# Performance work log

Measured on AMD Instinct MI355X. Metric: run time of the kernel, lower is better.

## Reference

```python
import jax, jax.numpy as jnp
import numpy as np

N_NODES = 100000
N_EDGES = 1600000
N_FEAT = 64
HIDDEN = 64
N_GRAPHS = 64
N_CLASSES = 2


def setup_inputs() -> dict:
    key = jax.random.key(0)
    ks = jax.random.split(key, 12)
    x = jax.random.normal(ks[0], (N_NODES, N_FEAT), dtype=jnp.float32)
    edge_index = jax.random.randint(ks[1], (2, N_EDGES), 0, N_NODES, dtype=jnp.int32)
    batch = jnp.sort(jax.random.randint(ks[2], (N_NODES,), 0, N_GRAPHS, dtype=jnp.int32))
    # Glorot-style init for GCNConv weights, zeros for biases (PyG default)
    def glorot(k, fan_in, fan_out):
        s = jnp.sqrt(6.0 / (fan_in + fan_out))
        return jax.random.uniform(k, (fan_in, fan_out), jnp.float32, -s, s)
    W1 = glorot(ks[3], N_FEAT, HIDDEN); b1 = jnp.zeros((HIDDEN,), jnp.float32)
    W2 = glorot(ks[4], HIDDEN, HIDDEN); b2 = jnp.zeros((HIDDEN,), jnp.float32)
    W3 = glorot(ks[5], HIDDEN, HIDDEN); b3 = jnp.zeros((HIDDEN,), jnp.float32)
    Wl = glorot(ks[6], HIDDEN, N_CLASSES); bl = jnp.zeros((N_CLASSES,), jnp.float32)
    return {"x": x, "edge_index": edge_index, "batch": batch,
            "W1": W1, "b1": b1, "W2": W2, "b2": b2, "W3": W3, "b3": b3,
            "Wl": Wl, "bl": bl}


def _gcn_conv(h, W, b, src, dst, dinv, n_nodes):
    # GCNConv with self-loops: out_i = sum_j d_i^-1/2 d_j^-1/2 (x_j W) + d_i^-1 (x_i W) + b
    h = h @ W                                   # [N, H]
    coef = (dinv[src] * dinv[dst])[:, None]     # [E, 1]
    agg = jax.ops.segment_sum(coef * h[src], dst, num_segments=n_nodes)
    return agg + (dinv * dinv)[:, None] * h + b


def reference(x, edge_index, batch, W1, b1, W2, b2, W3, b3, Wl, bl):
    src, dst = edge_index[0], edge_index[1]
    # degree of A + I (edge weight 1), shared by all three convs
    deg = jax.ops.segment_sum(jnp.ones((N_EDGES,), x.dtype), dst, num_segments=N_NODES) + 1.0
    dinv = jax.lax.rsqrt(deg)

    h = jax.nn.relu(_gcn_conv(x, W1, b1, src, dst, dinv, N_NODES))
    h = jax.nn.relu(_gcn_conv(h, W2, b2, src, dst, dinv, N_NODES))
    h = _gcn_conv(h, W3, b3, src, dst, dinv, N_NODES)

    # global_mean_pool over graph ids
    sums = jax.ops.segment_sum(h, batch, num_segments=N_GRAPHS)
    cnts = jax.ops.segment_sum(jnp.ones((N_NODES,), x.dtype), batch, num_segments=N_GRAPHS)
    pooled = sums / jnp.maximum(cnts, 1.0)[:, None]

    # dropout(p=0.5) is identity in eval mode
    return pooled @ Wl + bl
```

## Files before the change

kernel.cpp:

```cpp
#include <hip/hip_runtime.h>


#define NF 64
#define ELLW 64
#define BINSHIFT 9
#define BINW 512
#define NB 196
#define BINCAP 9216
#define LPITCH 68

typedef __attribute__((ext_vector_type(8))) short bf16x8;
typedef __attribute__((ext_vector_type(4))) float f32x4;

__device__ inline float bf2f(unsigned short u) {
    return __uint_as_float(((unsigned int)u) << 16);
}
__device__ inline float bf2f_lo(unsigned int u) {
    return __uint_as_float(u << 16);
}
__device__ inline float bf2f_hi(unsigned int u) {
    return __uint_as_float(u & 0xFFFF0000u);
}
__device__ inline unsigned short f2bf(float f) {
    unsigned int u = __float_as_uint(f);
    u = (u + 0x7fff + ((u >> 16) & 1)) >> 16;
    return (unsigned short)u;
}

__global__ void binA_kernel(const int* __restrict__ src, const int* __restrict__ dst,
                            int* __restrict__ binCnt, int* __restrict__ binEdges,
                            int nE, int chunk) {
    __shared__ int hist[NB];
    __shared__ int base[NB];
    int t = threadIdx.x;
    if (t < NB) hist[t] = 0;
    __syncthreads();
    int e0 = blockIdx.x * chunk;
    int e1 = min(e0 + chunk, nE);
    for (int e = e0 + t; e < e1; e += blockDim.x) {
        int b = dst[e] >> BINSHIFT;
        atomicAdd(&hist[b], 1);
    }
    __syncthreads();
    if (t < NB) {
        base[t] = atomicAdd(&binCnt[t], hist[t]);
        hist[t] = 0;
    }
    __syncthreads();
    for (int e = e0 + t; e < e1; e += blockDim.x) {
        int d = dst[e];
        int b = d >> BINSHIFT;
        int pos = base[b] + atomicAdd(&hist[b], 1);
        if (pos < BINCAP)
            binEdges[(size_t)b * BINCAP + pos] = src[e] | ((d & (BINW - 1)) << 17);
    }
}

__global__ void __launch_bounds__(512) binB_kernel(const int* __restrict__ binEdges,
                            const int* __restrict__ binCnt, int* __restrict__ cnt,
                            float* __restrict__ dinv, int* __restrict__ colELL, int n,
                            unsigned int* __restrict__ dummyA, unsigned int* __restrict__ dummyB) {
    __shared__ int lcnt[BINW];
    int t = threadIdx.x;
    int b = blockIdx.x;
    if (b == 0 && t < 32) { dummyA[t] = 0u; dummyB[t] = 0u; }
    for (int i = t; i < BINW; i += blockDim.x) lcnt[i] = 1;
    __syncthreads();
    int m = binCnt[b];
    if (m > BINCAP) m = BINCAP;
    const int* be = binEdges + (size_t)b * BINCAP;
    int nbase = b << BINSHIFT;
    for (int e = t; e < m; e += blockDim.x) {
        int v = be[e];
        int s = v & 0x1FFFF;
        int dl = v >> 17;
        int pos = atomicAdd(&lcnt[dl], 1);
        if (pos < ELLW) colELL[(size_t)(nbase + dl) * ELLW + pos] = s;
    }
    __syncthreads();
    for (int i = t; i < BINW; i += blockDim.x) {
        int node = nbase + i;
        if (node < n) {
            int c = lcnt[i];
            if (c > ELLW) c = ELLW;
            colELL[(size_t)node * ELLW + 0] = node;
            int cpad = (c + 3) & ~3;
            for (int j = c; j < cpad; ++j)
                colELL[(size_t)node * ELLW + j] = n;
            cnt[node] = c;
            dinv[node] = rsqrtf((float)c);
        }
    }
}

__device__ inline void load_W_frags(const float* __restrict__ W, int r16, int kq,
                                    bf16x8 bfr[4][2]) {
#pragma unroll
    for (int nt = 0; nt < 4; ++nt)
#pragma unroll
        for (int kh = 0; kh < 2; ++kh) {
            bf16x8 f;
#pragma unroll
            for (int j = 0; j < 8; ++j)
                f[j] = (short)f2bf(W[(kh * 32 + kq * 8 + j) * NF + nt * 16 + r16]);
            bfr[nt][kh] = f;
        }
}

__global__ void __launch_bounds__(256) gemm1_mfma_kernel(const float* __restrict__ A,
                                                         const float* __restrict__ W,
                                                         const float* __restrict__ dinv,
                                                         unsigned short* __restrict__ outB, int n) {
    __shared__ unsigned short T[4][16 * LPITCH];
    int lane = threadIdx.x & 63;
    int r16 = lane & 15, kq = lane >> 4;
    int wv = threadIdx.x >> 6;
    int wid = blockIdx.x * 4 + wv;
    int nw = gridDim.x * 4;
    bf16x8 bfr[4][2];
    load_W_frags(W, r16, kq, bfr);
    int ntiles = n >> 4;
    for (int t = wid; t < ntiles; t += nw) {
        int r0 = t << 4;
        const float* ar = A + (size_t)(r0 + r16) * NF + kq * 8;
        bf16x8 a0, a1;
        float4 v0 = *(const float4*)(ar);
        float4 v1 = *(const float4*)(ar + 4);
        float4 v2 = *(const float4*)(ar + 32);
        float4 v3 = *(const float4*)(ar + 36);
        a0[0] = (short)f2bf(v0.x); a0[1] = (short)f2bf(v0.y);
        a0[2] = (short)f2bf(v0.z); a0[3] = (short)f2bf(v0.w);
        a0[4] = (short)f2bf(v1.x); a0[5] = (short)f2bf(v1.y);
        a0[6] = (short)f2bf(v1.z); a0[7] = (short)f2bf(v1.w);
        a1[0] = (short)f2bf(v2.x); a1[1] = (short)f2bf(v2.y);
        a1[2] = (short)f2bf(v2.z); a1[3] = (short)f2bf(v2.w);
        a1[4] = (short)f2bf(v3.x); a1[5] = (short)f2bf(v3.y);
        a1[6] = (short)f2bf(v3.z); a1[7] = (short)f2bf(v3.w);
        f32x4 acc[4];
#pragma unroll
        for (int nt = 0; nt < 4; ++nt) {
            acc[nt] = (f32x4)(0.0f);
            acc[nt] = __builtin_amdgcn_mfma_f32_16x16x32_bf16(a0, bfr[nt][0], acc[nt], 0, 0, 0);
            acc[nt] = __builtin_amdgcn_mfma_f32_16x16x32_bf16(a1, bfr[nt][1], acc[nt], 0, 0, 0);
        }
        float ds[4];
#pragma unroll
        for (int reg = 0; reg < 4; ++reg) ds[reg] = dinv[r0 + kq * 4 + reg];
        unsigned short* Tw = T[wv];
#pragma unroll
        for (int nt = 0; nt < 4; ++nt)
#pragma unroll
            for (int reg = 0; reg < 4; ++reg)
                Tw[(kq * 4 + reg) * LPITCH + nt * 16 + r16] = f2bf(acc[nt][reg] * ds[reg]);
#pragma unroll
        for (int it = 0; it < 4; ++it) {
            int row = it * 4 + kq;
            uint2 v = *(const uint2*)&Tw[row * LPITCH + r16 * 4];
            *(uint2*)(outB + (size_t)(r0 + row) * NF + r16 * 4) = v;
        }
    }
}

__global__ void __launch_bounds__(256) fused_agg_gemm_kernel(
        const unsigned short* __restrict__ hB, const int* __restrict__ colELL,
        const int* __restrict__ cnt, const float* __restrict__ dinv,
        const float* __restrict__ bias, const float* __restrict__ W,
        unsigned short* __restrict__ outB, int n) {
    __shared__ int Icol[16 * 32];
    __shared__ int Icnt[16];
    __shared__ unsigned short Tin[2048];
    __shared__ unsigned short Tout[16 * LPITCH];
    int lane = threadIdx.x & 63;
    int wv = threadIdx.x >> 6;
    int es = lane >> 4, fq = lane & 15;
    int r16 = lane & 15, kq = lane >> 4;
    int r0 = blockIdx.x << 4;
    if (threadIdx.x < 128) {
        int srow = threadIdx.x >> 3, sj = threadIdx.x & 7;
        ((int4*)Icol)[srow * 8 + sj] =
            *(const int4*)(colELL + (size_t)(r0 + srow) * ELLW + sj * 4);
    } else if (threadIdx.x < 144) {
        Icnt[threadIdx.x - 128] = cnt[r0 + threadIdx.x - 128];
    }
    bf16x8 bfr0, bfr1;
    {
        bf16x8 f0, f1;
#pragma unroll
        for (int j = 0; j < 8; ++j) {
            f0[j] = (short)f2bf(W[(kq * 8 + j) * NF + wv * 16 + r16]);
            f1[j] = (short)f2bf(W[(32 + kq * 8 + j) * NF + wv * 16 + r16]);
        }
        bfr0 = f0; bfr1 = f1;
    }
    __syncthreads();
#pragma unroll
    for (int rr = 0; rr < 4; ++rr) {
        int lrow = wv * 4 + rr;
        int row = r0 + lrow;
        int c = Icnt[lrow];
        int nq = (c + 3) >> 2;
        int nqL = nq < 8 ? nq : 8;
        const int* cr = Icol + lrow * 32;
        float a0 = 0.f, a1 = 0.f, a2 = 0.f, a3 = 0.f;
        int q = 0;
        for (; q + 4 <= nqL; q += 4) {
            int s0 = cr[q * 4 + es];
            int s1 = cr[q * 4 + 4 + es];
            int s2 = cr[q * 4 + 8 + es];
            int s3 = cr[q * 4 + 12 + es];
            uint2 u0 = *(const uint2*)(hB + (size_t)s0 * NF + fq * 4);
            uint2 u1 = *(const uint2*)(hB + (size_t)s1 * NF + fq * 4);
            uint2 u2 = *(const uint2*)(hB + (size_t)s2 * NF + fq * 4);
            uint2 u3 = *(const uint2*)(hB + (size_t)s3 * NF + fq * 4);
            a0 += (bf2f_lo(u0.x) + bf2f_lo(u1.x)) + (bf2f_lo(u2.x) + bf2f_lo(u3.x));
            a1 += (bf2f_hi(u0.x) + bf2f_hi(u1.x)) + (bf2f_hi(u2.x) + bf2f_hi(u3.x));
            a2 += (bf2f_lo(u0.y) + bf2f_lo(u1.y)) + (bf2f_lo(u2.y) + bf2f_lo(u3.y));
            a3 += (bf2f_hi(u0.y) + bf2f_hi(u1.y)) + (bf2f_hi(u2.y) + bf2f_hi(u3.y));
        }
        for (; q + 2 <= nqL; q += 2) {
            int s0 = cr[q * 4 + es];
            int s1 = cr[q * 4 + 4 + es];
            uint2 u0 = *(const uint2*)(hB + (size_t)s0 * NF + fq * 4);
            uint2 u1 = *(const uint2*)(hB + (size_t)s1 * NF + fq * 4);
            a0 += bf2f_lo(u0.x) + bf2f_lo(u1.x);
            a1 += bf2f_hi(u0.x) + bf2f_hi(u1.x);
            a2 += bf2f_lo(u0.y) + bf2f_lo(u1.y);
            a3 += bf2f_hi(u0.y) + bf2f_hi(u1.y);
        }
        if (q < nqL) {
            int s0 = cr[q * 4 + es];
            uint2 u0 = *(const uint2*)(hB + (size_t)s0 * NF + fq * 4);
            a0 += bf2f_lo(u0.x); a1 += bf2f_hi(u0.x);
            a2 += bf2f_lo(u0.y); a3 += bf2f_hi(u0.y);
        }
        if (nq > 8) {
            const int* crg = colELL + (size_t)row * ELLW;
            for (int qq = 8; qq < nq; ++qq) {
                int s0 = crg[qq * 4 + es];
                uint2 u0 = *(const uint2*)(hB + (size_t)s0 * NF + fq * 4);
                a0 += bf2f_lo(u0.x); a1 += bf2f_hi(u0.x);
                a2 += bf2f_lo(u0.y); a3 += bf2f_hi(u0.y);
            }
        }
        a0 += __shfl_xor(a0, 16); a1 += __shfl_xor(a1, 16);
        a2 += __shfl_xor(a2, 16); a3 += __shfl_xor(a3, 16);
        a0 += __shfl_xor(a0, 32); a1 += __shfl_xor(a1, 32);
        a2 += __shfl_xor(a2, 32); a3 += __shfl_xor(a3, 32);
        if (es == 0) {
            float dd = dinv[row];
            float4 b4 = *(const float4*)(bias + fq * 4);
            a0 = fmaxf(dd * a0 + b4.x, 0.f); a1 = fmaxf(dd * a1 + b4.y, 0.f);
            a2 = fmaxf(dd * a2 + b4.z, 0.f); a3 = fmaxf(dd * a3 + b4.w, 0.f);
            uint2 v;
            v.x = (unsigned int)f2bf(a0) | ((unsigned int)f2bf(a1) << 16);
            v.y = (unsigned int)f2bf(a2) | ((unsigned int)f2bf(a3) << 16);
            int ibase = ((fq >> 3) << 10) + (((fq >> 1) & 3) << 7)
                      + (wv * 4 + rr) * 8 + ((fq & 1) << 2);
            *(uint2*)&Tin[ibase] = v;
        }
    }
    __syncthreads();
    bf16x8 A0 = *(const bf16x8*)&Tin[lane * 8];
    bf16x8 A1 = *(const bf16x8*)&Tin[1024 + lane * 8];
    f32x4 acc = (f32x4)(0.0f);
    acc = __builtin_amdgcn_mfma_f32_16x16x32_bf16(A0, bfr0, acc, 0, 0, 0);
    acc = __builtin_amdgcn_mfma_f32_16x16x32_bf16(A1, bfr1, acc, 0, 0, 0);
    float ds[4];
#pragma unroll
    for (int reg = 0; reg < 4; ++reg) ds[reg] = dinv[r0 + kq * 4 + reg];
#pragma unroll
    for (int reg = 0; reg < 4; ++reg)
        Tout[(kq * 4 + reg) * LPITCH + wv * 16 + r16] = f2bf(acc[reg] * ds[reg]);
    __syncthreads();
    int t = threadIdx.x;
    int orow = t >> 4, ocq = t & 15;
    uint2 v = *(const uint2*)&Tout[orow * LPITCH + ocq * 4];
    *(uint2*)(outB + (size_t)(r0 + orow) * NF + ocq * 4) = v;
}

__global__ void __launch_bounds__(256) gather3_kernel(
        const unsigned short* __restrict__ hB, const int* __restrict__ colELL,
        const int* __restrict__ cnt, const float* __restrict__ dinv,
        const float* __restrict__ bias, unsigned short* __restrict__ outB, int n) {
    __shared__ int Icol[16 * 32];
    __shared__ int Icnt[16];
    int lane = threadIdx.x & 63;
    int wv = threadIdx.x >> 6;
    int es = lane >> 4, fq = lane & 15;
    int r0 = blockIdx.x << 4;
    if (threadIdx.x < 128) {
        int srow = threadIdx.x >> 3, sj = threadIdx.x & 7;
        ((int4*)Icol)[srow * 8 + sj] =
            *(const int4*)(colELL + (size_t)(r0 + srow) * ELLW + sj * 4);
    } else if (threadIdx.x < 144) {
        Icnt[threadIdx.x - 128] = cnt[r0 + threadIdx.x - 128];
    }
    __syncthreads();
    float4 b4 = *(const float4*)(bias + fq * 4);
#pragma unroll
    for (int rr = 0; rr < 4; ++rr) {
        int lrow = wv * 4 + rr;
        int row = r0 + lrow;
        int c = Icnt[lrow];
        int nq = (c + 3) >> 2;
        int nqL = nq < 8 ? nq : 8;
        const int* cr = Icol + lrow * 32;
        float a0 = 0.f, a1 = 0.f, a2 = 0.f, a3 = 0.f;
        int q = 0;
        for (; q + 4 <= nqL; q += 4) {
            int s0 = cr[q * 4 + es];
            int s1 = cr[q * 4 + 4 + es];
            int s2 = cr[q * 4 + 8 + es];
            int s3 = cr[q * 4 + 12 + es];
            uint2 u0 = *(const uint2*)(hB + (size_t)s0 * NF + fq * 4);
            uint2 u1 = *(const uint2*)(hB + (size_t)s1 * NF + fq * 4);
            uint2 u2 = *(const uint2*)(hB + (size_t)s2 * NF + fq * 4);
            uint2 u3 = *(const uint2*)(hB + (size_t)s3 * NF + fq * 4);
            a0 += (bf2f_lo(u0.x) + bf2f_lo(u1.x)) + (bf2f_lo(u2.x) + bf2f_lo(u3.x));
            a1 += (bf2f_hi(u0.x) + bf2f_hi(u1.x)) + (bf2f_hi(u2.x) + bf2f_hi(u3.x));
            a2 += (bf2f_lo(u0.y) + bf2f_lo(u1.y)) + (bf2f_lo(u2.y) + bf2f_lo(u3.y));
            a3 += (bf2f_hi(u0.y) + bf2f_hi(u1.y)) + (bf2f_hi(u2.y) + bf2f_hi(u3.y));
        }
        for (; q + 2 <= nqL; q += 2) {
            int s0 = cr[q * 4 + es];
            int s1 = cr[q * 4 + 4 + es];
            uint2 u0 = *(const uint2*)(hB + (size_t)s0 * NF + fq * 4);
            uint2 u1 = *(const uint2*)(hB + (size_t)s1 * NF + fq * 4);
            a0 += bf2f_lo(u0.x) + bf2f_lo(u1.x);
            a1 += bf2f_hi(u0.x) + bf2f_hi(u1.x);
            a2 += bf2f_lo(u0.y) + bf2f_lo(u1.y);
            a3 += bf2f_hi(u0.y) + bf2f_hi(u1.y);
        }
        if (q < nqL) {
            int s0 = cr[q * 4 + es];
            uint2 u0 = *(const uint2*)(hB + (size_t)s0 * NF + fq * 4);
            a0 += bf2f_lo(u0.x); a1 += bf2f_hi(u0.x);
            a2 += bf2f_lo(u0.y); a3 += bf2f_hi(u0.y);
        }
        if (nq > 8) {
            const int* crg = colELL + (size_t)row * ELLW;
            for (int qq = 8; qq < nq; ++qq) {
                int s0 = crg[qq * 4 + es];
                uint2 u0 = *(const uint2*)(hB + (size_t)s0 * NF + fq * 4);
                a0 += bf2f_lo(u0.x); a1 += bf2f_hi(u0.x);
                a2 += bf2f_lo(u0.y); a3 += bf2f_hi(u0.y);
            }
        }
        a0 += __shfl_xor(a0, 16); a1 += __shfl_xor(a1, 16);
        a2 += __shfl_xor(a2, 16); a3 += __shfl_xor(a3, 16);
        a0 += __shfl_xor(a0, 32); a1 += __shfl_xor(a1, 32);
        a2 += __shfl_xor(a2, 32); a3 += __shfl_xor(a3, 32);
        if (es == 0) {
            float dd = dinv[row];
            float r0f = dd * a0 + b4.x, r1f = dd * a1 + b4.y;
            float r2f = dd * a2 + b4.z, r3f = dd * a3 + b4.w;
            uint2 v;
            v.x = (unsigned int)f2bf(r0f) | ((unsigned int)f2bf(r1f) << 16);
            v.y = (unsigned int)f2bf(r2f) | ((unsigned int)f2bf(r3f) << 16);
            *(uint2*)(outB + (size_t)row * NF + fq * 4) = v;
        }
    }
}

__global__ void __launch_bounds__(256) pool_kernel(const unsigned short* __restrict__ hB,
                            const int* __restrict__ batch,
                            float* __restrict__ pooled, int n) {
    const int CHUNK = 32;
    int wave = blockIdx.x * 4 + (threadIdx.x >> 6);
    int lane = threadIdx.x & 63;
    int start = wave * CHUNK;
    if (start >= n) return;
    int end = min(start + CHUNK, n);
    int gfirst = batch[start], glast = batch[end - 1];
    if (gfirst == glast && end - start == CHUNK) {
        float acc = 0.f;
#pragma unroll
        for (int r = 0; r < CHUNK; r += 8) {
            size_t base = (size_t)(start + r) * NF + lane;
            float v0 = bf2f(hB[base + 0 * NF]);
            float v1 = bf2f(hB[base + 1 * NF]);
            float v2 = bf2f(hB[base + 2 * NF]);
            float v3 = bf2f(hB[base + 3 * NF]);
            float v4 = bf2f(hB[base + 4 * NF]);
            float v5 = bf2f(hB[base + 5 * NF]);
            float v6 = bf2f(hB[base + 6 * NF]);
            float v7 = bf2f(hB[base + 7 * NF]);
            acc += ((v0 + v1) + (v2 + v3)) + ((v4 + v5) + (v6 + v7));
        }
        atomicAdd(&pooled[gfirst * NF + lane], acc);
    } else {
        int cur = gfirst;
        float acc = 0.f;
        for (int i = start; i < end; ++i) {
            int g = batch[i];
            if (g != cur) {
                atomicAdd(&pooled[cur * NF + lane], acc);
                acc = 0.f; cur = g;
            }
            acc += bf2f(hB[(size_t)i * NF + lane]);
        }
        atomicAdd(&pooled[cur * NF + lane], acc);
    }
}

__global__ void counts_kernel(const int* __restrict__ batch, float* __restrict__ counts, int n) {
    __shared__ int h[64];
    int t = threadIdx.x;
    if (t < 64) h[t] = 0;
    __syncthreads();
    for (int i = blockIdx.x * blockDim.x + t; i < n; i += gridDim.x * blockDim.x)
        atomicAdd(&h[batch[i]], 1);
    __syncthreads();
    if (t < 64 && h[t] > 0) atomicAdd(&counts[t], (float)h[t]);
}

__global__ void final_kernel(const float* __restrict__ pooled, const float* __restrict__ counts,
                             const float* __restrict__ Wl, const float* __restrict__ bl,
                             float* __restrict__ out) {
    int t = threadIdx.x;
    int g = t >> 1, c = t & 1;
    float inv = 1.0f / fmaxf(counts[g], 1.0f);
    float s = 0.0f;
#pragma unroll
    for (int j = 0; j < NF; ++j) s += pooled[g * NF + j] * Wl[j * 2 + c];
    out[t] = s * inv + bl[c];
}

extern "C" void kernel_launch(void* const* d_in, const int* in_sizes, int n_in,
                              void* d_out, int out_size, void* d_ws, size_t ws_size,
                              hipStream_t stream) {
    const float* x     = (const float*)d_in[0];
    const int*   ei    = (const int*)d_in[1];
    const int*   batch = (const int*)d_in[2];
    const float* W1    = (const float*)d_in[3];
    const float* b1    = (const float*)d_in[4];
    const float* W2    = (const float*)d_in[5];
    const float* b2    = (const float*)d_in[6];
    const float* W3    = (const float*)d_in[7];
    const float* b3    = (const float*)d_in[8];
    const float* Wl    = (const float*)d_in[9];
    const float* bl    = (const float*)d_in[10];
    float* out = (float*)d_out;

    const int n  = in_sizes[0] / NF;
    const int nE = in_sizes[1] / 2;
    const int* src = ei;
    const int* dst = ei + nE;

    char* ws = (char*)d_ws;
    auto alloc = [&](size_t bytes) {
        char* p = ws;
        ws += (bytes + 255) & ~(size_t)255;
        return p;
    };
    unsigned short* bufA = (unsigned short*)alloc((size_t)(n + 16) * NF * 2);
    unsigned short* bufB = (unsigned short*)alloc((size_t)(n + 16) * NF * 2);
    float* scratch = (float*)alloc((size_t)n * NF * 4);
    int*   binEdges = (int*)scratch;
    int*   colELL = (int*)alloc((size_t)n * ELLW * 4);
    float* dinv   = (float*)alloc((size_t)(n + 16) * 4);
    int*   cnt    = (int*)alloc((size_t)n * 4);
    char*  ztail  = ws;
    int*   binCnt = (int*)alloc(NB * 4);
    float* pooled = (float*)alloc(64 * NF * 4);
    float* counts = (float*)alloc(64 * 4);
    size_t zbytes = (size_t)(ws - ztail);

    hipMemsetAsync(ztail, 0, zbytes, stream);

    const int chunk = 3200;
    binA_kernel<<<(nE + chunk - 1) / chunk, 256, 0, stream>>>(src, dst, binCnt, binEdges, nE, chunk);
    binB_kernel<<<NB, 512, 0, stream>>>(binEdges, binCnt, cnt, dinv, colELL, n,
                                        (unsigned int*)(bufA + (size_t)n * NF),
                                        (unsigned int*)(bufB + (size_t)n * NF));
    counts_kernel<<<98, 1024, 0, stream>>>(batch, counts, n);

    const int tile_grid = n >> 4;

    gemm1_mfma_kernel<<<1563, 256, 0, stream>>>(x, W1, dinv, bufA, n);
    fused_agg_gemm_kernel<<<tile_grid, 256, 0, stream>>>(bufA, colELL, cnt, dinv, b1, W2, bufB, n);
    fused_agg_gemm_kernel<<<tile_grid, 256, 0, stream>>>(bufB, colELL, cnt, dinv, b2, W3, bufA, n);
    gather3_kernel<<<tile_grid, 256, 0, stream>>>(bufA, colELL, cnt, dinv, b3, bufB, n);

    pool_kernel<<<(n / 32 + 3) / 4, 256, 0, stream>>>(bufB, batch, pooled, n);
    final_kernel<<<1, 128, 0, stream>>>(pooled, counts, Wl, bl, out);
}
```

Before: 261.9 us.

## Switch intermediates to fp16, pre-convert weights, fuse layer-3 gather with pooling

Replaces bf16 storage and MFMA with fp16 across all layers, summing gathered neighbour rows with packed half adds before widening to float. A small prep kernel converts W1-W3 to fp16 once, so the GEMM kernels no longer round weights per block. The final gather kernel now accumulates the mean-pool sums directly through shared-memory and global atomics, which removes the layer-3 output write and the separate pool pass. The trade-off is reduced fp16 range and precision for partial sums, plus contention on the pooling atomics.

```diff
diff --git a/kernel.cpp b/kernel.cpp
--- a/kernel.cpp
+++ b/kernel.cpp
@@ -9,22 +9,16 @@
 #define BINCAP 9216
 #define LPITCH 68
 
-typedef __attribute__((ext_vector_type(8))) short bf16x8;
+typedef __attribute__((ext_vector_type(8))) _Float16 f16x8;
+typedef __attribute__((ext_vector_type(4))) _Float16 f16x4;
 typedef __attribute__((ext_vector_type(4))) float f32x4;
 
-__device__ inline float bf2f(unsigned short u) {
-    return __uint_as_float(((unsigned int)u) << 16);
-}
-__device__ inline float bf2f_lo(unsigned int u) {
-    return __uint_as_float(u << 16);
-}
-__device__ inline float bf2f_hi(unsigned int u) {
-    return __uint_as_float(u & 0xFFFF0000u);
-}
-__device__ inline unsigned short f2bf(float f) {
-    unsigned int u = __float_as_uint(f);
-    u = (u + 0x7fff + ((u >> 16) & 1)) >> 16;
-    return (unsigned short)u;
+__device__ inline unsigned short f2h_u(float f) {
+    return __builtin_bit_cast(unsigned short, (_Float16)f);
+}
+__device__ inline unsigned int pack_h2(float a, float b) {
+    unsigned int ua = f2h_u(a), ub = f2h_u(b);
+    return ua | (ub << 16);
 }
 
 __global__ void binA_kernel(const int* __restrict__ src, const int* __restrict__ dst,
@@ -93,22 +87,34 @@
     }
 }
 
-__device__ inline void load_W_frags(const float* __restrict__ W, int r16, int kq,
-                                    bf16x8 bfr[4][2]) {
+__global__ void prep_kernel(const float* __restrict__ W1, const float* __restrict__ W2,
+                            const float* __restrict__ W3, unsigned short* __restrict__ w1h,
+                            unsigned short* __restrict__ w2h, unsigned short* __restrict__ w3h) {
+    int t = blockIdx.x * blockDim.x + threadIdx.x;
+    if (t < NF * NF) {
+        w1h[t] = f2h_u(W1[t]);
+        w2h[t] = f2h_u(W2[t]);
+        w3h[t] = f2h_u(W3[t]);
+    }
+}
+
+__device__ inline void load_W_frags(const unsigned short* __restrict__ Wh, int r16, int kq,
+                                    f16x8 bfr[4][2]) {
 #pragma unroll
     for (int nt = 0; nt < 4; ++nt)
 #pragma unroll
         for (int kh = 0; kh < 2; ++kh) {
-            bf16x8 f;
+            f16x8 f;
 #pragma unroll
             for (int j = 0; j < 8; ++j)
-                f[j] = (short)f2bf(W[(kh * 32 + kq * 8 + j) * NF + nt * 16 + r16]);
+                f[j] = __builtin_bit_cast(_Float16,
+                        Wh[(kh * 32 + kq * 8 + j) * NF + nt * 16 + r16]);
             bfr[nt][kh] = f;
         }
 }
 
 __global__ void __launch_bounds__(256) gemm1_mfma_kernel(const float* __restrict__ A,
-                                                         const float* __restrict__ W,
+                                                         const unsigned short* __restrict__ Wh,
                                                          const float* __restrict__ dinv,
                                                          unsigned short* __restrict__ outB, int n) {
     __shared__ unsigned short T[4][16 * LPITCH];
@@ -117,31 +123,31 @@
     int wv = threadIdx.x >> 6;
     int wid = blockIdx.x * 4 + wv;
     int nw = gridDim.x * 4;
-    bf16x8 bfr[4][2];
-    load_W_frags(W, r16, kq, bfr);
+    f16x8 bfr[4][2];
+    load_W_frags(Wh, r16, kq, bfr);
     int ntiles = n >> 4;
     for (int t = wid; t < ntiles; t += nw) {
         int r0 = t << 4;
         const float* ar = A + (size_t)(r0 + r16) * NF + kq * 8;
-        bf16x8 a0, a1;
+        f16x8 a0, a1;
         float4 v0 = *(const float4*)(ar);
         float4 v1 = *(const float4*)(ar + 4);
         float4 v2 = *(const float4*)(ar + 32);
         float4 v3 = *(const float4*)(ar + 36);
-        a0[0] = (short)f2bf(v0.x); a0[1] = (short)f2bf(v0.y);
-        a0[2] = (short)f2bf(v0.z); a0[3] = (short)f2bf(v0.w);
-        a0[4] = (short)f2bf(v1.x); a0[5] = (short)f2bf(v1.y);
-        a0[6] = (short)f2bf(v1.z); a0[7] = (short)f2bf(v1.w);
-        a1[0] = (short)f2bf(v2.x); a1[1] = (short)f2bf(v2.y);
-        a1[2] = (short)f2bf(v2.z); a1[3] = (short)f2bf(v2.w);
-        a1[4] = (short)f2bf(v3.x); a1[5] = (short)f2bf(v3.y);
-        a1[6] = (short)f2bf(v3.z); a1[7] = (short)f2bf(v3.w);
+        a0[0] = (_Float16)v0.x; a0[1] = (_Float16)v0.y;
+        a0[2] = (_Float16)v0.z; a0[3] = (_Float16)v0.w;
+        a0[4] = (_Float16)v1.x; a0[5] = (_Float16)v1.y;
+        a0[6] = (_Float16)v1.z; a0[7] = (_Float16)v1.w;
+        a1[0] = (_Float16)v2.x; a1[1] = (_Float16)v2.y;
+        a1[2] = (_Float16)v2.z; a1[3] = (_Float16)v2.w;
+        a1[4] = (_Float16)v3.x; a1[5] = (_Float16)v3.y;
+        a1[6] = (_Float16)v3.z; a1[7] = (_Float16)v3.w;
         f32x4 acc[4];
 #pragma unroll
         for (int nt = 0; nt < 4; ++nt) {
             acc[nt] = (f32x4)(0.0f);
-            acc[nt] = __builtin_amdgcn_mfma_f32_16x16x32_bf16(a0, bfr[nt][0], acc[nt], 0, 0, 0);
-            acc[nt] = __builtin_amdgcn_mfma_f32_16x16x32_bf16(a1, bfr[nt][1], acc[nt], 0, 0, 0);
+            acc[nt] = __builtin_amdgcn_mfma_f32_16x16x32_f16(a0, bfr[nt][0], acc[nt], 0, 0, 0);
+            acc[nt] = __builtin_amdgcn_mfma_f32_16x16x32_f16(a1, bfr[nt][1], acc[nt], 0, 0, 0);
         }
         float ds[4];
 #pragma unroll
@@ -151,7 +157,7 @@
         for (int nt = 0; nt < 4; ++nt)
 #pragma unroll
             for (int reg = 0; reg < 4; ++reg)
-                Tw[(kq * 4 + reg) * LPITCH + nt * 16 + r16] = f2bf(acc[nt][reg] * ds[reg]);
+                Tw[(kq * 4 + reg) * LPITCH + nt * 16 + r16] = f2h_u(acc[nt][reg] * ds[reg]);
 #pragma unroll
         for (int it = 0; it < 4; ++it) {
             int row = it * 4 + kq;
@@ -164,7 +170,7 @@
 __global__ void __launch_bounds__(256) fused_agg_gemm_kernel(
         const unsigned short* __restrict__ hB, const int* __restrict__ colELL,
         const int* __restrict__ cnt, const float* __restrict__ dinv,
-        const float* __restrict__ bias, const float* __restrict__ W,
+        const float* __restrict__ bias, const unsigned short* __restrict__ Wh,
         unsigned short* __restrict__ outB, int n) {
     __shared__ int Icol[16 * 32];
     __shared__ int Icnt[16];
@@ -182,13 +188,13 @@
     } else if (threadIdx.x < 144) {
         Icnt[threadIdx.x - 128] = cnt[r0 + threadIdx.x - 128];
     }
-    bf16x8 bfr0, bfr1;
+    f16x8 bfr0, bfr1;
     {
-        bf16x8 f0, f1;
+        f16x8 f0, f1;
 #pragma unroll
         for (int j = 0; j < 8; ++j) {
-            f0[j] = (short)f2bf(W[(kq * 8 + j) * NF + wv * 16 + r16]);
-            f1[j] = (short)f2bf(W[(32 + kq * 8 + j) * NF + wv * 16 + r16]);
+            f0[j] = __builtin_bit_cast(_Float16, Wh[(kq * 8 + j) * NF + wv * 16 + r16]);
+            f1[j] = __builtin_bit_cast(_Float16, Wh[(32 + kq * 8 + j) * NF + wv * 16 + r16]);
         }
         bfr0 = f0; bfr1 = f1;
     }
@@ -208,38 +214,36 @@
             int s1 = cr[q * 4 + 4 + es];
             int s2 = cr[q * 4 + 8 + es];
             int s3 = cr[q * 4 + 12 + es];
-            uint2 u0 = *(const uint2*)(hB + (size_t)s0 * NF + fq * 4);
-            uint2 u1 = *(const uint2*)(hB + (size_t)s1 * NF + fq * 4);
-            uint2 u2 = *(const uint2*)(hB + (size_t)s2 * NF + fq * 4);
-            uint2 u3 = *(const uint2*)(hB + (size_t)s3 * NF + fq * 4);
-            a0 += (bf2f_lo(u0.x) + bf2f_lo(u1.x)) + (bf2f_lo(u2.x) + bf2f_lo(u3.x));
-            a1 += (bf2f_hi(u0.x) + bf2f_hi(u1.x)) + (bf2f_hi(u2.x) + bf2f_hi(u3.x));
-            a2 += (bf2f_lo(u0.y) + bf2f_lo(u1.y)) + (bf2f_lo(u2.y) + bf2f_lo(u3.y));
-            a3 += (bf2f_hi(u0.y) + bf2f_hi(u1.y)) + (bf2f_hi(u2.y) + bf2f_hi(u3.y));
+            f16x4 h0 = __builtin_bit_cast(f16x4, *(const uint2*)(hB + (size_t)s0 * NF + fq * 4));
+            f16x4 h1 = __builtin_bit_cast(f16x4, *(const uint2*)(hB + (size_t)s1 * NF + fq * 4));
+            f16x4 h2 = __builtin_bit_cast(f16x4, *(const uint2*)(hB + (size_t)s2 * NF + fq * 4));
+            f16x4 h3 = __builtin_bit_cast(f16x4, *(const uint2*)(hB + (size_t)s3 * NF + fq * 4));
+            f16x4 tt = (h0 + h1) + (h2 + h3);
+            a0 += (float)tt[0]; a1 += (float)tt[1];
+            a2 += (float)tt[2]; a3 += (float)tt[3];
         }
         for (; q + 2 <= nqL; q += 2) {
             int s0 = cr[q * 4 + es];
             int s1 = cr[q * 4 + 4 + es];
-            uint2 u0 = *(const uint2*)(hB + (size_t)s0 * NF + fq * 4);
-            uint2 u1 = *(const uint2*)(hB + (size_t)s1 * NF + fq * 4);
-            a0 += bf2f_lo(u0.x) + bf2f_lo(u1.x);
-            a1 += bf2f_hi(u0.x) + bf2f_hi(u1.x);
-            a2 += bf2f_lo(u0.y) + bf2f_lo(u1.y);
-            a3 += bf2f_hi(u0.y) + bf2f_hi(u1.y);
+            f16x4 h0 = __builtin_bit_cast(f16x4, *(const uint2*)(hB + (size_t)s0 * NF + fq * 4));
+            f16x4 h1 = __builtin_bit_cast(f16x4, *(const uint2*)(hB + (size_t)s1 * NF + fq * 4));
+            f16x4 tt = h0 + h1;
+            a0 += (float)tt[0]; a1 += (float)tt[1];
+            a2 += (float)tt[2]; a3 += (float)tt[3];
         }
         if (q < nqL) {
             int s0 = cr[q * 4 + es];
-            uint2 u0 = *(const uint2*)(hB + (size_t)s0 * NF + fq * 4);
-            a0 += bf2f_lo(u0.x); a1 += bf2f_hi(u0.x);
-            a2 += bf2f_lo(u0.y); a3 += bf2f_hi(u0.y);
+            f16x4 h0 = __builtin_bit_cast(f16x4, *(const uint2*)(hB + (size_t)s0 * NF + fq * 4));
+            a0 += (float)h0[0]; a1 += (float)h0[1];
+            a2 += (float)h0[2]; a3 += (float)h0[3];
         }
         if (nq > 8) {
             const int* crg = colELL + (size_t)row * ELLW;
             for (int qq = 8; qq < nq; ++qq) {
                 int s0 = crg[qq * 4 + es];
-                uint2 u0 = *(const uint2*)(hB + (size_t)s0 * NF + fq * 4);
-                a0 += bf2f_lo(u0.x); a1 += bf2f_hi(u0.x);
-                a2 += bf2f_lo(u0.y); a3 += bf2f_hi(u0.y);
+                f16x4 h0 = __builtin_bit_cast(f16x4, *(const uint2*)(hB + (size_t)s0 * NF + fq * 4));
+                a0 += (float)h0[0]; a1 += (float)h0[1];
+                a2 += (float)h0[2]; a3 += (float)h0[3];
             }
         }
         a0 += __shfl_xor(a0, 16); a1 += __shfl_xor(a1, 16);
@@ -252,25 +256,25 @@
             a0 = fmaxf(dd * a0 + b4.x, 0.f); a1 = fmaxf(dd * a1 + b4.y, 0.f);
             a2 = fmaxf(dd * a2 + b4.z, 0.f); a3 = fmaxf(dd * a3 + b4.w, 0.f);
             uint2 v;
-            v.x = (unsigned int)f2bf(a0) | ((unsigned int)f2bf(a1) << 16);
-            v.y = (unsigned int)f2bf(a2) | ((unsigned int)f2bf(a3) << 16);
+            v.x = pack_h2(a0, a1);
+            v.y = pack_h2(a2, a3);
             int ibase = ((fq >> 3) << 10) + (((fq >> 1) & 3) << 7)
                       + (wv * 4 + rr) * 8 + ((fq & 1) << 2);
             *(uint2*)&Tin[ibase] = v;
         }
     }
     __syncthreads();
-    bf16x8 A0 = *(const bf16x8*)&Tin[lane * 8];
-    bf16x8 A1 = *(const bf16x8*)&Tin[1024 + lane * 8];
+    f16x8 A0 = *(const f16x8*)&Tin[lane * 8];
+    f16x8 A1 = *(const f16x8*)&Tin[1024 + lane * 8];
     f32x4 acc = (f32x4)(0.0f);
-    acc = __builtin_amdgcn_mfma_f32_16x16x32_bf16(A0, bfr0, acc, 0, 0, 0);
-    acc = __builtin_amdgcn_mfma_f32_16x16x32_bf16(A1, bfr1, acc, 0, 0, 0);
+    acc = __builtin_amdgcn_mfma_f32_16x16x32_f16(A0, bfr0, acc, 0, 0, 0);
+    acc = __builtin_amdgcn_mfma_f32_16x16x32_f16(A1, bfr1, acc, 0, 0, 0);
     float ds[4];
 #pragma unroll
     for (int reg = 0; reg < 4; ++reg) ds[reg] = dinv[r0 + kq * 4 + reg];
 #pragma unroll
     for (int reg = 0; reg < 4; ++reg)
-        Tout[(kq * 4 + reg) * LPITCH + wv * 16 + r16] = f2bf(acc[reg] * ds[reg]);
+        Tout[(kq * 4 + reg) * LPITCH + wv * 16 + r16] = f2h_u(acc[reg] * ds[reg]);
     __syncthreads();
     int t = threadIdx.x;
     int orow = t >> 4, ocq = t & 15;
@@ -278,12 +282,14 @@
     *(uint2*)(outB + (size_t)(r0 + orow) * NF + ocq * 4) = v;
 }
 
-__global__ void __launch_bounds__(256) gather3_kernel(
+__global__ void __launch_bounds__(256) gather3_pool_kernel(
         const unsigned short* __restrict__ hB, const int* __restrict__ colELL,
         const int* __restrict__ cnt, const float* __restrict__ dinv,
-        const float* __restrict__ bias, unsigned short* __restrict__ outB, int n) {
+        const float* __restrict__ bias, const int* __restrict__ batch,
+        float* __restrict__ pooled, int n) {
     __shared__ int Icol[16 * 32];
     __shared__ int Icnt[16];
+    __shared__ float PL[2][NF];
     int lane = threadIdx.x & 63;
     int wv = threadIdx.x >> 6;
     int es = lane >> 4, fq = lane & 15;
@@ -292,10 +298,12 @@
         int srow = threadIdx.x >> 3, sj = threadIdx.x & 7;
         ((int4*)Icol)[srow * 8 + sj] =
             *(const int4*)(colELL + (size_t)(r0 + srow) * ELLW + sj * 4);
+        PL[threadIdx.x >> 6][threadIdx.x & 63] = 0.f;
     } else if (threadIdx.x < 144) {
         Icnt[threadIdx.x - 128] = cnt[r0 + threadIdx.x - 128];
     }
     __syncthreads();
+    int gb = batch[r0];
     float4 b4 = *(const float4*)(bias + fq * 4);
 #pragma unroll
     for (int rr = 0; rr < 4; ++rr) {
@@ -312,38 +320,36 @@
             int s1 = cr[q * 4 + 4 + es];
             int s2 = cr[q * 4 + 8 + es];
             int s3 = cr[q * 4 + 12 + es];
-            uint2 u0 = *(const uint2*)(hB + (size_t)s0 * NF + fq * 4);
-            uint2 u1 = *(const uint2*)(hB + (size_t)s1 * NF + fq * 4);
-            uint2 u2 = *(const uint2*)(hB + (size_t)s2 * NF + fq * 4);
-            uint2 u3 = *(const uint2*)(hB + (size_t)s3 * NF + fq * 4);
-            a0 += (bf2f_lo(u0.x) + bf2f_lo(u1.x)) + (bf2f_lo(u2.x) + bf2f_lo(u3.x));
-            a1 += (bf2f_hi(u0.x) + bf2f_hi(u1.x)) + (bf2f_hi(u2.x) + bf2f_hi(u3.x));
-            a2 += (bf2f_lo(u0.y) + bf2f_lo(u1.y)) + (bf2f_lo(u2.y) + bf2f_lo(u3.y));
-            a3 += (bf2f_hi(u0.y) + bf2f_hi(u1.y)) + (bf2f_hi(u2.y) + bf2f_hi(u3.y));
+            f16x4 h0 = __builtin_bit_cast(f16x4, *(const uint2*)(hB + (size_t)s0 * NF + fq * 4));
+            f16x4 h1 = __builtin_bit_cast(f16x4, *(const uint2*)(hB + (size_t)s1 * NF + fq * 4));
+            f16x4 h2 = __builtin_bit_cast(f16x4, *(const uint2*)(hB + (size_t)s2 * NF + fq * 4));
+            f16x4 h3 = __builtin_bit_cast(f16x4, *(const uint2*)(hB + (size_t)s3 * NF + fq * 4));
+            f16x4 tt = (h0 + h1) + (h2 + h3);
+            a0 += (float)tt[0]; a1 += (float)tt[1];
+            a2 += (float)tt[2]; a3 += (float)tt[3];
         }
         for (; q + 2 <= nqL; q += 2) {
             int s0 = cr[q * 4 + es];
             int s1 = cr[q * 4 + 4 + es];
-            uint2 u0 = *(const uint2*)(hB + (size_t)s0 * NF + fq * 4);
-            uint2 u1 = *(const uint2*)(hB + (size_t)s1 * NF + fq * 4);
-            a0 += bf2f_lo(u0.x) + bf2f_lo(u1.x);
-            a1 += bf2f_hi(u0.x) + bf2f_hi(u1.x);
-            a2 += bf2f_lo(u0.y) + bf2f_lo(u1.y);
-            a3 += bf2f_hi(u0.y) + bf2f_hi(u1.y);
+            f16x4 h0 = __builtin_bit_cast(f16x4, *(const uint2*)(hB + (size_t)s0 * NF + fq * 4));
+            f16x4 h1 = __builtin_bit_cast(f16x4, *(const uint2*)(hB + (size_t)s1 * NF + fq * 4));
+            f16x4 tt = h0 + h1;
+            a0 += (float)tt[0]; a1 += (float)tt[1];
+            a2 += (float)tt[2]; a3 += (float)tt[3];
         }
         if (q < nqL) {
             int s0 = cr[q * 4 + es];
-            uint2 u0 = *(const uint2*)(hB + (size_t)s0 * NF + fq * 4);
-            a0 += bf2f_lo(u0.x); a1 += bf2f_hi(u0.x);
-            a2 += bf2f_lo(u0.y); a3 += bf2f_hi(u0.y);
+            f16x4 h0 = __builtin_bit_cast(f16x4, *(const uint2*)(hB + (size_t)s0 * NF + fq * 4));
+            a0 += (float)h0[0]; a1 += (float)h0[1];
+            a2 += (float)h0[2]; a3 += (float)h0[3];
         }
         if (nq > 8) {
             const int* crg = colELL + (size_t)row * ELLW;
             for (int qq = 8; qq < nq; ++qq) {
                 int s0 = crg[qq * 4 + es];
-                uint2 u0 = *(const uint2*)(hB + (size_t)s0 * NF + fq * 4);
-                a0 += bf2f_lo(u0.x); a1 += bf2f_hi(u0.x);
-                a2 += bf2f_lo(u0.y); a3 += bf2f_hi(u0.y);
+                f16x4 h0 = __builtin_bit_cast(f16x4, *(const uint2*)(hB + (size_t)s0 * NF + fq * 4));
+                a0 += (float)h0[0]; a1 += (float)h0[1];
+                a2 += (float)h0[2]; a3 += (float)h0[3];
             }
         }
         a0 += __shfl_xor(a0, 16); a1 += __shfl_xor(a1, 16);
@@ -354,52 +360,26 @@
             float dd = dinv[row];
             float r0f = dd * a0 + b4.x, r1f = dd * a1 + b4.y;
             float r2f = dd * a2 + b4.z, r3f = dd * a3 + b4.w;
-            uint2 v;
-            v.x = (unsigned int)f2bf(r0f) | ((unsigned int)f2bf(r1f) << 16);
-            v.y = (unsigned int)f2bf(r2f) | ((unsigned int)f2bf(r3f) << 16);
-            *(uint2*)(outB + (size_t)row * NF + fq * 4) = v;
-        }
-    }
-}
-
-__global__ void __launch_bounds__(256) pool_kernel(const unsigned short* __restrict__ hB,
-                            const int* __restrict__ batch,
-                            float* __restrict__ pooled, int n) {
-    const int CHUNK = 32;
-    int wave = blockIdx.x * 4 + (threadIdx.x >> 6);
-    int lane = threadIdx.x & 63;
-    int start = wave * CHUNK;
-    if (start >= n) return;
-    int end = min(start + CHUNK, n);
-    int gfirst = batch[start], glast = batch[end - 1];
-    if (gfirst == glast && end - start == CHUNK) {
-        float acc = 0.f;
-#pragma unroll
-        for (int r = 0; r < CHUNK; r += 8) {
-            size_t base = (size_t)(start + r) * NF + lane;
-            float v0 = bf2f(hB[base + 0 * NF]);
-            float v1 = bf2f(hB[base + 1 * NF]);
-            float v2 = bf2f(hB[base + 2 * NF]);
-            float v3 = bf2f(hB[base + 3 * NF]);
-            float v4 = bf2f(hB[base + 4 * NF]);
-            float v5 = bf2f(hB[base + 5 * NF]);
-            float v6 = bf2f(hB[base + 6 * NF]);
-            float v7 = bf2f(hB[base + 7 * NF]);
-            acc += ((v0 + v1) + (v2 + v3)) + ((v4 + v5) + (v6 + v7));
-        }
-        atomicAdd(&pooled[gfirst * NF + lane], acc);
-    } else {
-        int cur = gfirst;
-        float acc = 0.f;
-        for (int i = start; i < end; ++i) {
-            int g = batch[i];
-            if (g != cur) {
-                atomicAdd(&pooled[cur * NF + lane], acc);
-                acc = 0.f; cur = g;
+            int g = batch[row];
+            int sel = g - gb;
+            if (sel < 2) {
+                atomicAdd(&PL[sel][fq * 4 + 0], r0f);
+                atomicAdd(&PL[sel][fq * 4 + 1], r1f);
+                atomicAdd(&PL[sel][fq * 4 + 2], r2f);
+                atomicAdd(&PL[sel][fq * 4 + 3], r3f);
+            } else {
+                atomicAdd(&pooled[g * NF + fq * 4 + 0], r0f);
+                atomicAdd(&pooled[g * NF + fq * 4 + 1], r1f);
+                atomicAdd(&pooled[g * NF + fq * 4 + 2], r2f);
+                atomicAdd(&pooled[g * NF + fq * 4 + 3], r3f);
             }
-            acc += bf2f(hB[(size_t)i * NF + lane]);
-        }
-        atomicAdd(&pooled[cur * NF + lane], acc);
+        }
+    }
+    __syncthreads();
+    if (threadIdx.x < 128) {
+        int s = threadIdx.x >> 6, f = threadIdx.x & 63;
+        float v = PL[s][f];
+        if (v != 0.f) atomicAdd(&pooled[(gb + s) * NF + f], v);
     }
 }
 
@@ -460,6 +440,9 @@
     int*   colELL = (int*)alloc((size_t)n * ELLW * 4);
     float* dinv   = (float*)alloc((size_t)(n + 16) * 4);
     int*   cnt    = (int*)alloc((size_t)n * 4);
+    unsigned short* w1h = (unsigned short*)alloc((size_t)NF * NF * 2);
+    unsigned short* w2h = (unsigned short*)alloc((size_t)NF * NF * 2);
+    unsigned short* w3h = (unsigned short*)alloc((size_t)NF * NF * 2);
     char*  ztail  = ws;
     int*   binCnt = (int*)alloc(NB * 4);
     float* pooled = (float*)alloc(64 * NF * 4);
@@ -474,14 +457,14 @@
                                         (unsigned int*)(bufA + (size_t)n * NF),
                                         (unsigned int*)(bufB + (size_t)n * NF));
     counts_kernel<<<98, 1024, 0, stream>>>(batch, counts, n);
+    prep_kernel<<<16, 256, 0, stream>>>(W1, W2, W3, w1h, w2h, w3h);
 
     const int tile_grid = n >> 4;
 
-    gemm1_mfma_kernel<<<1563, 256, 0, stream>>>(x, W1, dinv, bufA, n);
-    fused_agg_gemm_kernel<<<tile_grid, 256, 0, stream>>>(bufA, colELL, cnt, dinv, b1, W2, bufB, n);
-    fused_agg_gemm_kernel<<<tile_grid, 256, 0, stream>>>(bufB, colELL, cnt, dinv, b2, W3, bufA, n);
-    gather3_kernel<<<tile_grid, 256, 0, stream>>>(bufA, colELL, cnt, dinv, b3, bufB, n);
-
-    pool_kernel<<<(n / 32 + 3) / 4, 256, 0, stream>>>(bufB, batch, pooled, n);
+    gemm1_mfma_kernel<<<1563, 256, 0, stream>>>(x, w1h, dinv, bufA, n);
+    fused_agg_gemm_kernel<<<tile_grid, 256, 0, stream>>>(bufA, colELL, cnt, dinv, b1, w2h, bufB, n);
+    fused_agg_gemm_kernel<<<tile_grid, 256, 0, stream>>>(bufB, colELL, cnt, dinv, b2, w3h, bufA, n);
+    gather3_pool_kernel<<<tile_grid, 256, 0, stream>>>(bufA, colELL, cnt, dinv, b3, batch, pooled, n);
+
     final_kernel<<<1, 128, 0, stream>>>(pooled, counts, Wl, bl, out);
 }
```

After: 258.8 us. No clear change (-1.2%).
